# Kernel optimization log

Hardware: AMD Instinct MI355X
Metric: run time of the kernel (lower is better)

## Reference

```python
import jax, jax.numpy as jnp
import numpy as np

B = 4096
N_BLOCK = 100
N_SLOT = 300
N_YS = 1236
HID = 256
STEPS = 100
NEG = -1000.0


def _init_w(key, shape):
    # uniform(-1/sqrt(fan_in), 1/sqrt(fan_in)) like torch Linear/LSTMCell
    fan = shape[-1]
    return jax.random.uniform(key, shape, jnp.float32, -1.0, 1.0) / jnp.sqrt(jnp.float32(fan))


def setup_inputs() -> dict:
    key = jax.random.key(0)
    ks = jax.random.split(key, 16)
    to_tensor = jax.random.uniform(ks[0], (B, N_BLOCK, 5), jnp.float32)
    ti_tensor = jax.random.uniform(ks[1], (B, N_BLOCK, 5), jnp.float32)
    ys_tensor = jax.random.uniform(ks[2], (B, N_YS, 5), jnp.float32)
    # many slots are feasible, count starts at 5 so the decrement/zero-out logic is exercised.
    dims = jax.random.uniform(ks[3], (B, N_SLOT, 4), jnp.float32) * 2.0
    count = jnp.full((B, N_SLOT, 1), 5.0, jnp.float32)
    slot_info = jnp.concatenate([dims, count], axis=-1)
    params = dict(
        W1=_init_w(ks[4], (512, 1436)), b1=jnp.zeros(512, jnp.float32),
        W2=_init_w(ks[5], (512, 512)), b2=jnp.zeros(512, jnp.float32),
        W3=_init_w(ks[6], (256, 512)), b3=jnp.zeros(256, jnp.float32),
        W_fe2=_init_w(ks[7], (1, 5)), b_fe2=jnp.zeros(1, jnp.float32),
        Wih_to=_init_w(ks[8], (4 * HID, 5)), Whh_to=_init_w(ks[9], (4 * HID, HID)),
        bih_to=jnp.zeros(4 * HID, jnp.float32), bhh_to=jnp.zeros(4 * HID, jnp.float32),
        Wih_ti=_init_w(ks[10], (4 * HID, 5)), Whh_ti=_init_w(ks[11], (4 * HID, HID)),
        bih_ti=jnp.zeros(4 * HID, jnp.float32), bhh_ti=jnp.zeros(4 * HID, jnp.float32),
        Wb=_init_w(ks[12], (N_BLOCK, HID)), bb=jnp.zeros(N_BLOCK, jnp.float32),
        Ws=_init_w(ks[13], (N_SLOT, HID)), bs=jnp.zeros(N_SLOT, jnp.float32),
    )
    return {"to_tensor": to_tensor, "ti_tensor": ti_tensor, "ys_tensor": ys_tensor,
            "slot_info": slot_info, **params}


def _lstm(x, h, c, Wih, Whh, bih, bhh):
    g = x @ Wih.T + bih + h @ Whh.T + bhh  # [B, 4H]
    i, f, gg, o = jnp.split(g, 4, axis=-1)  # torch gate order: i, f, g, o
    c = jax.nn.sigmoid(f) * c + jax.nn.sigmoid(i) * jnp.tanh(gg)
    h = jax.nn.sigmoid(o) * jnp.tanh(c)
    return h, c


def reference(to_tensor, ti_tensor, ys_tensor, slot_info,
              W1, b1, W2, b2, W3, b3, W_fe2, b_fe2,
              Wih_to, Whh_to, bih_to, bhh_to,
              Wih_ti, Whh_ti, bih_ti, bhh_ti,
              Wb, bb, Ws, bs):
    state = jnp.concatenate([to_tensor, ti_tensor, ys_tensor], axis=1)  # [B,1436,5]
    x = state.transpose(0, 2, 1)                    # [B,5,1436]
    x = jax.nn.relu(x @ W1.T + b1)                  # Dropout is identity in eval mode
    x = jax.nn.relu(x @ W2.T + b2)
    x = jax.nn.relu(x @ W3.T + b3)                  # [B,5,256]
    feat_vec = (x.transpose(0, 2, 1) @ W_fe2.T + b_fe2)[..., 0]  # [B,256]

    bsz = to_tensor.shape[0]
    batch_idx = jnp.arange(bsz)
    zeros5 = jnp.zeros((bsz, 5), to_tensor.dtype)   # input_ti is never updated in the loop
    mask_to0 = to_tensor[:, :, 0] != -1.0
    mask_ti0 = ti_tensor[:, :, 0] != -1.0
    carry0 = (feat_vec, jnp.zeros((bsz, HID), jnp.float32),
              feat_vec, jnp.zeros((bsz, HID), jnp.float32),
              zeros5, mask_to0, mask_ti0, slot_info)

    def step(carry, _):
        h_to, c_to, h_ti, c_ti, inp_to, m_to, m_ti, slots = carry
        h_to, c_to = _lstm(inp_to, h_to, c_to, Wih_to, Whh_to, bih_to, bhh_to)
        # masked block logits; argmax of softmax == argmax of masked logits
        logit_b = jnp.where(m_to, h_to @ Wb.T + bb, NEG)
        sel_b = jnp.argmax(logit_b, axis=-1)                      # [B]
        inp_to = jnp.take_along_axis(to_tensor, sel_b[:, None, None], axis=1)[:, 0, :]  # [B,5]
        m_to = m_to.at[batch_idx, sel_b].set(False)
        # slot feasibility: block (l,w) must be strictly smaller than slot (l,w), slot nonempty
        slot_mask = jnp.any(inp_to[:, None, :2] >= slots[:, :, :2], axis=-1) | (slots[:, :, 0] == 0.0)
        logit_s = jnp.where(slot_mask, NEG, h_to @ Ws.T + bs)
        sel_s = jnp.argmax(logit_s, axis=-1)
        slots = slots.at[batch_idx, sel_s, 4].add(-1.0)
        slots = jnp.where((slots[:, :, 4] == 0.0)[:, :, None], 0.0, slots)
        h_ti, c_ti = _lstm(zeros5, h_ti, c_ti, Wih_ti, Whh_ti, bih_ti, bhh_ti)
        logit_bti = jnp.where(m_ti, h_ti @ Wb.T + bb, NEG)
        sel_bti = jnp.argmax(logit_bti, axis=-1)
        m_ti = m_ti.at[batch_idx, sel_bti].set(False)
        out = jnp.stack([sel_b, sel_s, sel_bti], axis=-1)         # [B,3]
        return (h_to, c_to, h_ti, c_ti, inp_to, m_to, m_ti, slots), out

    _, acts = jax.lax.scan(step, carry0, None, length=STEPS)      # [100,B,3]
    actions = acts.transpose(1, 0, 2)                             # [B,100,3]
    return state, actions
```

## Files before the change

### kernel.cpp

```cpp
#include <hip/hip_runtime.h>
#include <cstddef>

#define BATCH   4096
#define NBLK    100
#define NSLOT   300
#define NSTATE  1436
#define HID     256
#define NSTEPS  100
#define NEGV    (-1000.0f)
#define KC      384


__device__ __forceinline__ float sigf(float x) {
#pragma clang fp contract(off)
  float e = (float)exp(-(double)x);
  float d = 1.0f + e;
  return 1.0f / d;
}
__device__ __forceinline__ float tanhf32(float x) {
  return (float)tanh((double)x);
}

__device__ __forceinline__ void argmax64f(float& v, int& i) {
#pragma unroll
  for (int off = 32; off > 0; off >>= 1) {
    float v2 = __shfl_down(v, off, 64);
    int   i2 = __shfl_down(i, off, 64);
    if (v2 > v || (v2 == v && i2 < i)) { v = v2; i = i2; }
  }
  v = __shfl(v, 0, 64);
  i = __shfl(i, 0, 64);
}

__global__ __launch_bounds__(256) void concat_kernel(
    const float* __restrict__ to_t, const float* __restrict__ ti_t,
    const float* __restrict__ ys_t, float* __restrict__ state)
{
  int b = blockIdx.x;
  for (int li = threadIdx.x; li < 7180; li += 256) {
    float v = (li < 500)  ? to_t[(size_t)b * 500 + li]
            : (li < 1000) ? ti_t[(size_t)b * 500 + (li - 500)]
                          : ys_t[(size_t)b * 6180 + (li - 1000)];
    state[(size_t)b * 7180 + li] = v;
  }
}

__device__ __forceinline__ void gemm32_tile(
    const float* __restrict__ A, int lda,
    const float* __restrict__ W, int ldw,
    const float* __restrict__ bias,
    float* __restrict__ C, int ldc,
    int N, int K, int row0, int col0, bool relu)
{
#pragma clang fp contract(off)
  __shared__ float As[16][68];
  __shared__ float Ws[16][68];
  const int t = threadIdx.x;
  const int tx = t & 15, ty = t >> 4;
  const int mload = t >> 2;
  const int kq    = (t & 3) << 2;
  const int gn    = col0 + mload;
  const float* Aptr = A + (size_t)(row0 + mload) * lda + kq;
  const float* Wptr = (gn < N) ? (W + (size_t)gn * ldw + kq) : nullptr;

  float acc[4][4] = {};
  float res[4][4];
  bool first = true;
  for (int k0 = 0; k0 < K; k0 += 16) {
    if (k0 > 0 && (k0 % KC) == 0) {
#pragma unroll
      for (int i = 0; i < 4; i++)
#pragma unroll
        for (int j = 0; j < 4; j++) {
          res[i][j] = first ? acc[i][j] : (res[i][j] + acc[i][j]);
          acc[i][j] = 0.0f;
        }
      first = false;
    }
    float4 av = *(const float4*)(Aptr + k0);
    float4 wv = make_float4(0.f, 0.f, 0.f, 0.f);
    if (Wptr) wv = *(const float4*)(Wptr + k0);
    As[kq + 0][mload] = av.x; As[kq + 1][mload] = av.y;
    As[kq + 2][mload] = av.z; As[kq + 3][mload] = av.w;
    Ws[kq + 0][mload] = wv.x; Ws[kq + 1][mload] = wv.y;
    Ws[kq + 2][mload] = wv.z; Ws[kq + 3][mload] = wv.w;
    __syncthreads();
#pragma unroll
    for (int kk = 0; kk < 16; kk++) {
      float a[4], w[4];
#pragma unroll
      for (int i = 0; i < 4; i++) { a[i] = As[kk][ty * 4 + i]; w[i] = Ws[kk][tx * 4 + i]; }
#pragma unroll
      for (int i = 0; i < 4; i++)
#pragma unroll
        for (int j = 0; j < 4; j++) acc[i][j] = fmaf(a[i], w[j], acc[i][j]);
    }
    __syncthreads();
  }
#pragma unroll
  for (int i = 0; i < 4; i++)
#pragma unroll
    for (int j = 0; j < 4; j++)
      res[i][j] = first ? acc[i][j] : (res[i][j] + acc[i][j]);

#pragma unroll
  for (int i = 0; i < 4; i++) {
    size_t row = (size_t)(row0 + ty * 4 + i) * ldc;
#pragma unroll
    for (int j = 0; j < 4; j++) {
      int n = col0 + tx * 4 + j;
      if (n < N) {
        float v = res[i][j] + bias[n];
        if (relu) v = v > 0.0f ? v : 0.0f;
        C[row + n] = v;
      }
    }
  }
}

__global__ __launch_bounds__(256) void gemm32_kernel(
    const float* __restrict__ A, int lda, const float* __restrict__ W, int ldw,
    const float* __restrict__ bias, float* __restrict__ C, int ldc,
    int N, int K, int relu)
{
  gemm32_tile(A, lda, W, ldw, bias, C, ldc, N, K,
              blockIdx.y * 64, blockIdx.x * 64, relu != 0);
}

__global__ __launch_bounds__(256) void gemm1_kernel(
    const float* __restrict__ state, const float* __restrict__ W1,
    const float* __restrict__ b1, float* __restrict__ X1, int row_base)
{
#pragma clang fp contract(off)
  __shared__ float As[16][68];
  __shared__ float Ws[16][68];
  const int t = threadIdx.x;
  const int tx = t & 15, ty = t >> 4;
  const int mload = t >> 2;
  const int kq    = (t & 3) << 2;
  const int row0 = blockIdx.y * 64, col0 = blockIdx.x * 64;
  const int R = row_base + row0 + mload;
  const int b = R / 5, j = R - b * 5;
  const float* sp = state + (size_t)b * 7180 + j;
  const float* Wptr = W1 + (size_t)(col0 + mload) * NSTATE + kq;

  float acc[4][4] = {};
  float res[4][4];
  bool first = true;
  for (int k0 = 0; k0 < 1440; k0 += 16) {
    if (k0 == 384 || k0 == 768 || k0 == 1152) {
#pragma unroll
      for (int i = 0; i < 4; i++)
#pragma unroll
        for (int jj = 0; jj < 4; jj++) {
          res[i][jj] = first ? acc[i][jj] : (res[i][jj] + acc[i][jj]);
          acc[i][jj] = 0.0f;
        }
      first = false;
    }
    int n = k0 + kq;
    float a0 = (n + 0 < NSTATE) ? sp[(n + 0) * 5] : 0.0f;
    float a1 = (n + 1 < NSTATE) ? sp[(n + 1) * 5] : 0.0f;
    float a2 = (n + 2 < NSTATE) ? sp[(n + 2) * 5] : 0.0f;
    float a3 = (n + 3 < NSTATE) ? sp[(n + 3) * 5] : 0.0f;
    float4 wv = make_float4(0.f, 0.f, 0.f, 0.f);
    if (n + 3 < NSTATE) wv = *(const float4*)(Wptr + k0);
    As[kq + 0][mload] = a0; As[kq + 1][mload] = a1;
    As[kq + 2][mload] = a2; As[kq + 3][mload] = a3;
    Ws[kq + 0][mload] = wv.x; Ws[kq + 1][mload] = wv.y;
    Ws[kq + 2][mload] = wv.z; Ws[kq + 3][mload] = wv.w;
    __syncthreads();
#pragma unroll
    for (int kk = 0; kk < 16; kk++) {
      float a[4], w[4];
#pragma unroll
      for (int i = 0; i < 4; i++) { a[i] = As[kk][ty * 4 + i]; w[i] = Ws[kk][tx * 4 + i]; }
#pragma unroll
      for (int i = 0; i < 4; i++)
#pragma unroll
        for (int jj = 0; jj < 4; jj++) acc[i][jj] = fmaf(a[i], w[jj], acc[i][jj]);
    }
    __syncthreads();
  }
#pragma unroll
  for (int i = 0; i < 4; i++)
#pragma unroll
    for (int jj = 0; jj < 4; jj++)
      res[i][jj] = res[i][jj] + acc[i][jj];

#pragma unroll
  for (int i = 0; i < 4; i++) {
    size_t row = (size_t)(row0 + ty * 4 + i) * 512;
#pragma unroll
    for (int jj = 0; jj < 4; jj++) {
      int n = col0 + tx * 4 + jj;
      float v = res[i][jj] + b1[n];
      X1[row + n] = v > 0.0f ? v : 0.0f;
    }
  }
}

__global__ __launch_bounds__(256) void feat2c_kernel(
    const float* __restrict__ X3, const float* __restrict__ W_fe2,
    const float* __restrict__ b_fe2, float* __restrict__ hto,
    float* __restrict__ cto, float* __restrict__ hti, float* __restrict__ cti,
    int b_base)
{
#pragma clang fp contract(off)
  int bl = blockIdx.x, b = b_base + bl, k = threadIdx.x;
  float s = 0.0f;
#pragma unroll
  for (int j = 0; j < 5; j++)
    s = fmaf(X3[((size_t)bl * 5 + j) * 256 + k], W_fe2[j], s);
  float acc = s + b_fe2[0];
  hto[(size_t)b * 256 + k] = acc;
  hti[(size_t)b * 256 + k] = acc;
  cto[(size_t)b * 256 + k] = 0.0f;
  cti[(size_t)b * 256 + k] = 0.0f;
}

__global__ __launch_bounds__(320) void init_state_kernel(
    const float* __restrict__ to_t, const float* __restrict__ ti_t,
    const float* __restrict__ slot_info, float* __restrict__ slots,
    int* __restrict__ m_to, int* __restrict__ m_ti, float* __restrict__ inp)
{
  int b = blockIdx.x, t = threadIdx.x;
  for (int li = t; li < NSLOT * 5; li += 320)
    slots[(size_t)b * (NSLOT * 5) + li] = slot_info[(size_t)b * (NSLOT * 5) + li];
  if (t < NBLK) {
    m_to[b * 128 + t] = (to_t[(size_t)b * 500 + t * 5] != -1.0f) ? 1 : 0;
    m_ti[b * 128 + t] = (ti_t[(size_t)b * 500 + t * 5] != -1.0f) ? 1 : 0;
  }
  if (t < 8) inp[b * 8 + t] = 0.0f;
}

__global__ __launch_bounds__(256) void init_weights_kernel(
    const float* __restrict__ Wb, const float* __restrict__ bb,
    const float* __restrict__ Ws, const float* __restrict__ bs,
    float* __restrict__ Wcat, float* __restrict__ bcat)
{
  int idx = blockIdx.x * 256 + threadIdx.x;
  if (idx < 400 * 256) {
    int n = idx / 256, k = idx % 256;
    Wcat[idx] = (n < 100) ? Wb[n * 256 + k] : Ws[(n - 100) * 256 + k];
  }
  if (idx < 400) bcat[idx] = (idx < 100) ? bb[idx] : bs[idx - 100];
}

__global__ __launch_bounds__(256) void gates_kernel(
    const float* __restrict__ h, const float* __restrict__ Whh,
    const float* __restrict__ Wih, const float* __restrict__ bih,
    const float* __restrict__ bhh, const float* __restrict__ inp,
    float* __restrict__ g)
{
#pragma clang fp contract(off)
  __shared__ float As[16][68];
  __shared__ float Ws[16][68];
  const int t = threadIdx.x;
  const int tx = t & 15, ty = t >> 4;
  const int mload = t >> 2;
  const int kq    = (t & 3) << 2;
  const int row0 = blockIdx.y * 64, col0 = blockIdx.x * 64;
  const float* Aptr = h + (size_t)(row0 + mload) * 256 + kq;
  const float* Wptr = Whh + (size_t)(col0 + mload) * 256 + kq;

  float acc[4][4] = {};
  for (int k0 = 0; k0 < 256; k0 += 16) {
    float4 av = *(const float4*)(Aptr + k0);
    float4 wv = *(const float4*)(Wptr + k0);
    As[kq + 0][mload] = av.x; As[kq + 1][mload] = av.y;
    As[kq + 2][mload] = av.z; As[kq + 3][mload] = av.w;
    Ws[kq + 0][mload] = wv.x; Ws[kq + 1][mload] = wv.y;
    Ws[kq + 2][mload] = wv.z; Ws[kq + 3][mload] = wv.w;
    __syncthreads();
#pragma unroll
    for (int kk = 0; kk < 16; kk++) {
      float a[4], w[4];
#pragma unroll
      for (int i = 0; i < 4; i++) { a[i] = As[kk][ty * 4 + i]; w[i] = Ws[kk][tx * 4 + i]; }
#pragma unroll
      for (int i = 0; i < 4; i++)
#pragma unroll
        for (int j = 0; j < 4; j++) acc[i][j] = fmaf(a[i], w[j], acc[i][j]);
    }
    __syncthreads();
  }

  float wih[4][5], bihv[4], bhhv[4];
#pragma unroll
  for (int j = 0; j < 4; j++) {
    int o = col0 + tx * 4 + j;
#pragma unroll
    for (int k = 0; k < 5; k++) wih[j][k] = Wih[o * 5 + k];
    bihv[j] = bih[o];
    bhhv[j] = bhh[o];
  }
#pragma unroll
  for (int i = 0; i < 4; i++) {
    int r = row0 + ty * 4 + i;
    float xv[5];
    if (inp) {
#pragma unroll
      for (int k = 0; k < 5; k++) xv[k] = inp[r * 8 + k];
    } else {
#pragma unroll
      for (int k = 0; k < 5; k++) xv[k] = 0.0f;
    }
    size_t row = (size_t)r * 1024;
#pragma unroll
    for (int j = 0; j < 4; j++) {
      float ih = 0.0f;
#pragma unroll
      for (int k = 0; k < 5; k++) ih = fmaf(xv[k], wih[j][k], ih);
      float v1 = ih + bihv[j];
      float v2 = v1 + acc[i][j];
      float v3 = v2 + bhhv[j];
      g[row + j + tx * 4 + col0 - (tx * 4 + j) + (tx * 4 + j)] = v3;
    }
  }
}

__global__ __launch_bounds__(256) void lstm32_kernel(
    const float* __restrict__ g, float* __restrict__ h, float* __restrict__ c)
{
#pragma clang fp contract(off)
  int b = blockIdx.x, u = threadIdx.x;
  const float* gr = g + (size_t)b * 1024;
  float i_ = gr[u], f_ = gr[256 + u], gg = gr[512 + u], o_ = gr[768 + u];
  float sf = sigf(f_);
  float si = sigf(i_);
  float tg = tanhf32(gg);
  float t2 = sf * c[(size_t)b * 256 + u];
  float t5 = si * tg;
  float cc = t2 + t5;
  c[(size_t)b * 256 + u] = cc;
  float so = sigf(o_);
  float tc = tanhf32(cc);
  h[(size_t)b * 256 + u] = so * tc;
}

__global__ __launch_bounds__(256) void logits32_kernel(
    const float* __restrict__ hto, const float* __restrict__ hti,
    const float* __restrict__ Wcat, const float* __restrict__ bcat,
    const float* __restrict__ Wb, const float* __restrict__ bb,
    float* __restrict__ L)
{
  int ct = blockIdx.x;
  if (ct < 7)
    gemm32_tile(hto, 256, Wcat, 256, bcat, L, 512, 400, 256,
                blockIdx.y * 64, ct * 64, false);
  else
    gemm32_tile(hti, 256, Wb, 256, bb, L + 400, 512, 100, 256,
                blockIdx.y * 64, (ct - 7) * 64, false);
}

__global__ __launch_bounds__(64) void select32_kernel(
    const float* __restrict__ L, const float* __restrict__ to_t,
    int* __restrict__ m_to, int* __restrict__ m_ti, float* __restrict__ slots,
    float* __restrict__ inp, float* __restrict__ out_act, int step)
{
  int b = blockIdx.x, lane = threadIdx.x;
  const float* Lr = L + (size_t)b * 512;

  float bv = -3.4e38f; int bi = 0x7fffffff;
  for (int n = lane; n < NBLK; n += 64) {
    float v = m_to[b * 128 + n] ? Lr[n] : NEGV;
    if (v > bv) { bv = v; bi = n; }
  }
  argmax64f(bv, bi);
  int sel_b = bi;
  const float* blk = to_t + (size_t)b * 500 + sel_b * 5;
  float i0 = blk[0], i1 = blk[1];
  if (lane == 0) m_to[b * 128 + sel_b] = 0;
  if (lane < 5) inp[b * 8 + lane] = blk[lane];

  float sv = -3.4e38f; int si = 0x7fffffff;
  float* sl = slots + (size_t)b * (NSLOT * 5);
  for (int s = lane; s < NSLOT; s += 64) {
    float l = sl[s * 5 + 0], w = sl[s * 5 + 1];
    bool mask = (i0 >= l) || (i1 >= w) || (l == 0.0f);
    float v = mask ? NEGV : Lr[100 + s];
    if (v > sv) { sv = v; si = s; }
  }
  argmax64f(sv, si);
  int sel_s = si;
  if (lane == 0) {
    float c = sl[sel_s * 5 + 4] - 1.0f;
    if (c == 0.0f) {
      sl[sel_s * 5 + 0] = 0.f; sl[sel_s * 5 + 1] = 0.f; sl[sel_s * 5 + 2] = 0.f;
      sl[sel_s * 5 + 3] = 0.f; sl[sel_s * 5 + 4] = 0.f;
    } else {
      sl[sel_s * 5 + 4] = c;
    }
  }

  float tv = -3.4e38f; int tii = 0x7fffffff;
  for (int n = lane; n < NBLK; n += 64) {
    float v = m_ti[b * 128 + n] ? Lr[400 + n] : NEGV;
    if (v > tv) { tv = v; tii = n; }
  }
  argmax64f(tv, tii);
  if (lane == 0) {
    m_ti[b * 128 + tii] = 0;
    float* oa = out_act + (size_t)b * (NSTEPS * 3) + step * 3;
    oa[0] = (float)sel_b; oa[1] = (float)sel_s; oa[2] = (float)tii;
  }
}

extern "C" void kernel_launch(void* const* d_in, const int* in_sizes, int n_in,
                              void* d_out, int out_size, void* d_ws, size_t ws_size,
                              hipStream_t stream) {
  (void)in_sizes; (void)n_in; (void)out_size; (void)ws_size;
  const float* to_t   = (const float*)d_in[0];
  const float* ti_t   = (const float*)d_in[1];
  const float* ys_t   = (const float*)d_in[2];
  const float* slot_i = (const float*)d_in[3];
  const float* W1 = (const float*)d_in[4];  const float* b1 = (const float*)d_in[5];
  const float* W2 = (const float*)d_in[6];  const float* b2 = (const float*)d_in[7];
  const float* W3 = (const float*)d_in[8];  const float* b3 = (const float*)d_in[9];
  const float* W_fe2 = (const float*)d_in[10]; const float* b_fe2 = (const float*)d_in[11];
  const float* Wih_to = (const float*)d_in[12]; const float* Whh_to = (const float*)d_in[13];
  const float* bih_to = (const float*)d_in[14]; const float* bhh_to = (const float*)d_in[15];
  const float* Wih_ti = (const float*)d_in[16]; const float* Whh_ti = (const float*)d_in[17];
  const float* bih_ti = (const float*)d_in[18]; const float* bhh_ti = (const float*)d_in[19];
  const float* Wb = (const float*)d_in[20]; const float* bb = (const float*)d_in[21];
  const float* Ws = (const float*)d_in[22]; const float* bs = (const float*)d_in[23];

  float* outf      = (float*)d_out;
  float* state_out = outf;
  float* out_act   = outf + (size_t)BATCH * NSTATE * 5;

  float* ws = (float*)d_ws;
  float* X1 = ws;
  float* X2 = ws + 1310720;
  float* X3 = ws + 2621440;
  float* g  = ws;
  float* Lb = ws + 4194304;
  float* hto = ws + 6291456;
  float* hti = ws + 7340032;
  float* cto = ws + 8388608;
  float* cti = ws + 9437184;
  float* slots = ws + 10485760;
  int*   m_to  = (int*)(ws + 16629760);
  int*   m_ti  = (int*)(ws + 17154048);
  float* inp_buf = ws + 17678336;
  float* Wcat  = ws + 17711104;
  float* bcat  = ws + 17813504;

  concat_kernel<<<dim3(BATCH), 256, 0, stream>>>(to_t, ti_t, ys_t, state_out);
  init_state_kernel<<<dim3(BATCH), 320, 0, stream>>>(to_t, ti_t, slot_i, slots,
                                                     m_to, m_ti, inp_buf);
  init_weights_kernel<<<dim3(400), 256, 0, stream>>>(Wb, bb, Ws, bs, Wcat, bcat);

  for (int c = 0; c < 8; c++) {
    int rb = c * 2560, b0 = c * 512;
    gemm1_kernel<<<dim3(8, 40), 256, 0, stream>>>(state_out, W1, b1, X1, rb);
    gemm32_kernel<<<dim3(8, 40), 256, 0, stream>>>(X1, 512, W2, 512, b2,
                                                   X2, 512, 512, 512, 1);
    gemm32_kernel<<<dim3(4, 40), 256, 0, stream>>>(X2, 512, W3, 512, b3,
                                                   X3, 256, 256, 512, 1);
    feat2c_kernel<<<dim3(512), 256, 0, stream>>>(X3, W_fe2, b_fe2,
                                                 hto, cto, hti, cti, b0);
  }

  for (int s = 0; s < NSTEPS; s++) {
    gates_kernel<<<dim3(16, 64), 256, 0, stream>>>(hto, Whh_to, Wih_to,
                                                   bih_to, bhh_to, inp_buf, g);
    lstm32_kernel<<<dim3(BATCH), 256, 0, stream>>>(g, hto, cto);
    gates_kernel<<<dim3(16, 64), 256, 0, stream>>>(hti, Whh_ti, Wih_ti,
                                                   bih_ti, bhh_ti, nullptr, g);
    lstm32_kernel<<<dim3(BATCH), 256, 0, stream>>>(g, hti, cti);
    logits32_kernel<<<dim3(9, 64), 256, 0, stream>>>(hto, hti, Wcat, bcat, Wb, bb, Lb);
    select32_kernel<<<dim3(BATCH), 64, 0, stream>>>(Lb, to_t, m_to, m_ti, slots,
                                                    inp_buf, out_act, s);
  }
}
```

Before: 16.02 ms.

## Fuse LSTM gate GEMM with cell update and batch both LSTMs in one launch

Merges the gate GEMM and the elementwise LSTM cell update into one kernel. Each block computes all four gates (i,f,g,o) for 64 hidden units, so the cell update can run in registers, and the 4096x1024 gate buffer no longer goes through global memory. The to and ti LSTMs run in a single launch along the z grid dimension, and h is double-buffered so blocks never read h values that other blocks are overwriting. This cuts four launches per step to one and removes the gate round trip, in exchange for a 64-element accumulator per thread, more shared memory and fewer blocks per step.

```diff
diff --git a/kernel.cpp b/kernel.cpp
--- a/kernel.cpp
+++ b/kernel.cpp
@@ -247,96 +247,118 @@
   if (idx < 400) bcat[idx] = (idx < 100) ? bb[idx] : bs[idx - 100];
 }
 
-__global__ __launch_bounds__(256) void gates_kernel(
-    const float* __restrict__ h, const float* __restrict__ Whh,
-    const float* __restrict__ Wih, const float* __restrict__ bih,
-    const float* __restrict__ bhh, const float* __restrict__ inp,
-    float* __restrict__ g)
+__global__ __launch_bounds__(256, 2) void gates_lstm_kernel(
+    const float* __restrict__ hin_to, const float* __restrict__ hin_ti,
+    float* __restrict__ hout_to, float* __restrict__ hout_ti,
+    float* __restrict__ cto, float* __restrict__ cti,
+    const float* __restrict__ Whh_to, const float* __restrict__ Wih_to,
+    const float* __restrict__ bih_to, const float* __restrict__ bhh_to,
+    const float* __restrict__ Whh_ti,
+    const float* __restrict__ bih_ti, const float* __restrict__ bhh_ti,
+    const float* __restrict__ inp)
 {
 #pragma clang fp contract(off)
-  __shared__ float As[16][68];
-  __shared__ float Ws[16][68];
-  const int t = threadIdx.x;
+  __shared__ float As[32][68];
+  __shared__ float Wsh[32][272];
+  const bool is_to = (blockIdx.z == 0);
+  const float* __restrict__ h_in  = is_to ? hin_to : hin_ti;
+  float* __restrict__ h_out = is_to ? hout_to : hout_ti;
+  float* __restrict__ cbuf  = is_to ? cto : cti;
+  const float* __restrict__ Whh = is_to ? Whh_to : Whh_ti;
+  const float* __restrict__ bih = is_to ? bih_to : bih_ti;
+  const float* __restrict__ bhh = is_to ? bhh_to : bhh_ti;
+
+  const int t  = threadIdx.x;
   const int tx = t & 15, ty = t >> 4;
-  const int mload = t >> 2;
-  const int kq    = (t & 3) << 2;
-  const int row0 = blockIdx.y * 64, col0 = blockIdx.x * 64;
-  const float* Aptr = h + (size_t)(row0 + mload) * 256 + kq;
-  const float* Wptr = Whh + (size_t)(col0 + mload) * 256 + kq;
-
-  float acc[4][4] = {};
-  for (int k0 = 0; k0 < 256; k0 += 16) {
-    float4 av = *(const float4*)(Aptr + k0);
-    float4 wv = *(const float4*)(Wptr + k0);
-    As[kq + 0][mload] = av.x; As[kq + 1][mload] = av.y;
-    As[kq + 2][mload] = av.z; As[kq + 3][mload] = av.w;
-    Ws[kq + 0][mload] = wv.x; Ws[kq + 1][mload] = wv.y;
-    Ws[kq + 2][mload] = wv.z; Ws[kq + 3][mload] = wv.w;
+  const int u0   = blockIdx.x * 64;
+  const int row0 = blockIdx.y * 64;
+  const int rr   = t >> 3;
+  const int kq8  = (t & 7) << 2;
+
+  float acc[4][4][4] = {};
+
+  for (int k0 = 0; k0 < 256; k0 += 32) {
+#pragma unroll
+    for (int p = 0; p < 2; p++) {
+      int r = p * 32 + rr;
+      float4 v = *(const float4*)(h_in + (size_t)(row0 + r) * 256 + k0 + kq8);
+      As[kq8 + 0][r] = v.x; As[kq8 + 1][r] = v.y;
+      As[kq8 + 2][r] = v.z; As[kq8 + 3][r] = v.w;
+    }
+#pragma unroll
+    for (int p = 0; p < 8; p++) {
+      int r = p * 32 + rr;
+      int q = r >> 6, c = r & 63;
+      float4 v = *(const float4*)(Whh + (size_t)(q * 256 + u0 + c) * 256 + k0 + kq8);
+      Wsh[kq8 + 0][q * 68 + c] = v.x; Wsh[kq8 + 1][q * 68 + c] = v.y;
+      Wsh[kq8 + 2][q * 68 + c] = v.z; Wsh[kq8 + 3][q * 68 + c] = v.w;
+    }
     __syncthreads();
 #pragma unroll
-    for (int kk = 0; kk < 16; kk++) {
-      float a[4], w[4];
-#pragma unroll
-      for (int i = 0; i < 4; i++) { a[i] = As[kk][ty * 4 + i]; w[i] = Ws[kk][tx * 4 + i]; }
-#pragma unroll
-      for (int i = 0; i < 4; i++)
-#pragma unroll
-        for (int j = 0; j < 4; j++) acc[i][j] = fmaf(a[i], w[j], acc[i][j]);
+    for (int kk = 0; kk < 32; kk++) {
+      float4 a4 = *(const float4*)&As[kk][ty * 4];
+      float a[4] = {a4.x, a4.y, a4.z, a4.w};
+#pragma unroll
+      for (int q = 0; q < 4; q++) {
+        float4 w4 = *(const float4*)&Wsh[kk][q * 68 + tx * 4];
+        float w[4] = {w4.x, w4.y, w4.z, w4.w};
+#pragma unroll
+        for (int i = 0; i < 4; i++)
+#pragma unroll
+          for (int j = 0; j < 4; j++)
+            acc[q][i][j] = fmaf(a[i], w[j], acc[q][i][j]);
+      }
     }
     __syncthreads();
   }
 
-  float wih[4][5], bihv[4], bhhv[4];
-#pragma unroll
-  for (int j = 0; j < 4; j++) {
-    int o = col0 + tx * 4 + j;
-#pragma unroll
-    for (int k = 0; k < 5; k++) wih[j][k] = Wih[o * 5 + k];
-    bihv[j] = bih[o];
-    bhhv[j] = bhh[o];
-  }
+  float xv[4][5];
 #pragma unroll
   for (int i = 0; i < 4; i++) {
     int r = row0 + ty * 4 + i;
-    float xv[5];
-    if (inp) {
-#pragma unroll
-      for (int k = 0; k < 5; k++) xv[k] = inp[r * 8 + k];
-    } else {
-#pragma unroll
-      for (int k = 0; k < 5; k++) xv[k] = 0.0f;
-    }
-    size_t row = (size_t)r * 1024;
-#pragma unroll
-    for (int j = 0; j < 4; j++) {
-      float ih = 0.0f;
-#pragma unroll
-      for (int k = 0; k < 5; k++) ih = fmaf(xv[k], wih[j][k], ih);
-      float v1 = ih + bihv[j];
-      float v2 = v1 + acc[i][j];
-      float v3 = v2 + bhhv[j];
-      g[row + j + tx * 4 + col0 - (tx * 4 + j) + (tx * 4 + j)] = v3;
-    }
-  }
-}
-
-__global__ __launch_bounds__(256) void lstm32_kernel(
-    const float* __restrict__ g, float* __restrict__ h, float* __restrict__ c)
-{
-#pragma clang fp contract(off)
-  int b = blockIdx.x, u = threadIdx.x;
-  const float* gr = g + (size_t)b * 1024;
-  float i_ = gr[u], f_ = gr[256 + u], gg = gr[512 + u], o_ = gr[768 + u];
-  float sf = sigf(f_);
-  float si = sigf(i_);
-  float tg = tanhf32(gg);
-  float t2 = sf * c[(size_t)b * 256 + u];
-  float t5 = si * tg;
-  float cc = t2 + t5;
-  c[(size_t)b * 256 + u] = cc;
-  float so = sigf(o_);
-  float tc = tanhf32(cc);
-  h[(size_t)b * 256 + u] = so * tc;
+#pragma unroll
+    for (int k5 = 0; k5 < 5; k5++)
+      xv[i][k5] = is_to ? inp[r * 8 + k5] : 0.0f;
+  }
+#pragma unroll
+  for (int j = 0; j < 4; j++) {
+    int u = u0 + tx * 4 + j;
+    float gv[4][4];
+#pragma unroll
+    for (int q = 0; q < 4; q++) {
+      int o = q * 256 + u;
+      float bihv = bih[o], bhhv = bhh[o];
+      float wih[5];
+#pragma unroll
+      for (int k5 = 0; k5 < 5; k5++) wih[k5] = is_to ? Wih_to[o * 5 + k5] : 0.0f;
+#pragma unroll
+      for (int i = 0; i < 4; i++) {
+        float ih = 0.0f;
+#pragma unroll
+        for (int k5 = 0; k5 < 5; k5++) ih = fmaf(xv[i][k5], wih[k5], ih);
+        float v1 = ih + bihv;
+        float v2 = v1 + acc[q][i][j];
+        float v3 = v2 + bhhv;
+        gv[q][i] = v3;
+      }
+    }
+#pragma unroll
+    for (int i = 0; i < 4; i++) {
+      int r = row0 + ty * 4 + i;
+      float i_ = gv[0][i], f_ = gv[1][i], gg = gv[2][i], o_ = gv[3][i];
+      float sf = sigf(f_);
+      float si = sigf(i_);
+      float tg = tanhf32(gg);
+      float cp = cbuf[(size_t)r * 256 + u];
+      float t2 = sf * cp;
+      float t5 = si * tg;
+      float cc = t2 + t5;
+      cbuf[(size_t)r * 256 + u] = cc;
+      float so = sigf(o_);
+      float tc = tanhf32(cc);
+      h_out[(size_t)r * 256 + u] = so * tc;
+    }
+  }
 }
 
 __global__ __launch_bounds__(256) void logits32_kernel(
@@ -421,7 +443,7 @@
   const float* W_fe2 = (const float*)d_in[10]; const float* b_fe2 = (const float*)d_in[11];
   const float* Wih_to = (const float*)d_in[12]; const float* Whh_to = (const float*)d_in[13];
   const float* bih_to = (const float*)d_in[14]; const float* bhh_to = (const float*)d_in[15];
-  const float* Wih_ti = (const float*)d_in[16]; const float* Whh_ti = (const float*)d_in[17];
+  const float* Whh_ti = (const float*)d_in[17];
   const float* bih_ti = (const float*)d_in[18]; const float* bhh_ti = (const float*)d_in[19];
   const float* Wb = (const float*)d_in[20]; const float* bb = (const float*)d_in[21];
   const float* Ws = (const float*)d_in[22]; const float* bs = (const float*)d_in[23];
@@ -431,21 +453,22 @@
   float* out_act   = outf + (size_t)BATCH * NSTATE * 5;
 
   float* ws = (float*)d_ws;
-  float* X1 = ws;
-  float* X2 = ws + 1310720;
-  float* X3 = ws + 2621440;
-  float* g  = ws;
-  float* Lb = ws + 4194304;
-  float* hto = ws + 6291456;
-  float* hti = ws + 7340032;
-  float* cto = ws + 8388608;
-  float* cti = ws + 9437184;
-  float* slots = ws + 10485760;
-  int*   m_to  = (int*)(ws + 16629760);
-  int*   m_ti  = (int*)(ws + 17154048);
-  float* inp_buf = ws + 17678336;
-  float* Wcat  = ws + 17711104;
-  float* bcat  = ws + 17813504;
+  float* Lb    = ws;
+  float* hA_to = ws + 2097152;
+  float* hA_ti = ws + 3145728;
+  float* hB_to = ws + 4194304;
+  float* hB_ti = ws + 5242880;
+  float* cto   = ws + 6291456;
+  float* cti   = ws + 7340032;
+  float* slots = ws + 8388608;
+  int*   m_to  = (int*)(ws + 14532608);
+  int*   m_ti  = (int*)(ws + 15056896);
+  float* inp_buf = ws + 15581184;
+  float* Wcat  = ws + 15613952;
+  float* bcat  = ws + 15716352;
+  float* X1    = ws + 15720448;
+  float* X2    = ws + 17031168;
+  float* X3    = ws + 18341888;
 
   concat_kernel<<<dim3(BATCH), 256, 0, stream>>>(to_t, ti_t, ys_t, state_out);
   init_state_kernel<<<dim3(BATCH), 320, 0, stream>>>(to_t, ti_t, slot_i, slots,
@@ -460,17 +483,19 @@
     gemm32_kernel<<<dim3(4, 40), 256, 0, stream>>>(X2, 512, W3, 512, b3,
                                                    X3, 256, 256, 512, 1);
     feat2c_kernel<<<dim3(512), 256, 0, stream>>>(X3, W_fe2, b_fe2,
-                                                 hto, cto, hti, cti, b0);
+                                                 hA_to, cto, hA_ti, cti, b0);
   }
 
   for (int s = 0; s < NSTEPS; s++) {
-    gates_kernel<<<dim3(16, 64), 256, 0, stream>>>(hto, Whh_to, Wih_to,
-                                                   bih_to, bhh_to, inp_buf, g);
-    lstm32_kernel<<<dim3(BATCH), 256, 0, stream>>>(g, hto, cto);
-    gates_kernel<<<dim3(16, 64), 256, 0, stream>>>(hti, Whh_ti, Wih_ti,
-                                                   bih_ti, bhh_ti, nullptr, g);
-    lstm32_kernel<<<dim3(BATCH), 256, 0, stream>>>(g, hti, cti);
-    logits32_kernel<<<dim3(9, 64), 256, 0, stream>>>(hto, hti, Wcat, bcat, Wb, bb, Lb);
+    const float* hin_to = (s & 1) ? hB_to : hA_to;
+    const float* hin_ti = (s & 1) ? hB_ti : hA_ti;
+    float* hout_to = (s & 1) ? hA_to : hB_to;
+    float* hout_ti = (s & 1) ? hA_ti : hB_ti;
+    gates_lstm_kernel<<<dim3(4, 64, 2), 256, 0, stream>>>(
+        hin_to, hin_ti, hout_to, hout_ti, cto, cti,
+        Whh_to, Wih_to, bih_to, bhh_to, Whh_ti, bih_ti, bhh_ti, inp_buf);
+    logits32_kernel<<<dim3(9, 64), 256, 0, stream>>>(hout_to, hout_ti,
+                                                     Wcat, bcat, Wb, bb, Lb);
     select32_kernel<<<dim3(BATCH), 64, 0, stream>>>(Lb, to_t, m_to, m_ti, slots,
                                                     inp_buf, out_act, s);
   }
```

Result: slower. 19.74 ms (+23.2%).
